# Performance work log

Measured on AMD Instinct MI355X. Metric: run time of the kernel, lower is better.

Reference implementation:

```python
import jax, jax.numpy as jnp
import numpy as np

H = 4096          # hidden_size
NIN = 17          # RFSIZE*RFSIZE + ADDINPUT + NBACTIONS = 9+4+4
NA = 4            # NBACTIONS


def setup_inputs() -> dict:
    key = jax.random.key(0)
    ks = jax.random.split(key, 12)
    return {
        "x": jax.random.normal(ks[0], (1, NIN), jnp.float32),
        "hidden": 0.1 * jax.random.normal(ks[1], (1, H), jnp.float32),
        "hebb": 0.01 * jax.random.normal(ks[2], (H, H), jnp.float32),
        "i2h_w": 0.1 * jax.random.normal(ks[3], (H, NIN), jnp.float32),
        "i2h_b": 0.1 * jax.random.normal(ks[4], (H,), jnp.float32),
        "w": 0.01 * jax.random.uniform(ks[5], (H, H), jnp.float32),
        "alpha": 0.01 * jax.random.uniform(ks[6], (H, H), jnp.float32),
        "eta": 0.01 * jnp.ones((1,), jnp.float32),
        "h2o_w": 0.1 * jax.random.normal(ks[7], (NA, H), jnp.float32),
        "h2o_b": 0.1 * jax.random.normal(ks[8], (NA,), jnp.float32),
        "h2v_w": 0.1 * jax.random.normal(ks[9], (1, H), jnp.float32),
        "h2v_b": 0.1 * jax.random.normal(ks[10], (1,), jnp.float32),
    }


def reference(x, hidden, hebb, i2h_w, i2h_b, w, alpha, eta, h2o_w, h2o_b, h2v_w, h2v_b):
    # plastic RNN step: h = tanh(i2h(x) + hidden @ (w + alpha*hebb))
    h = jnp.tanh(x @ i2h_w.T + i2h_b + hidden @ (w + alpha * hebb))  # [1,H]
    # Hebbian trace update: (1-eta)*hebb + eta * outer(hidden, h)
    hebb_new = (1.0 - eta) * hebb + eta * (hidden[0][:, None] * h[0][None, :])  # [H,H]
    activout = jax.nn.softmax(h @ h2o_w.T + h2o_b, axis=-1)  # [1,NA]
    valueout = h @ h2v_w.T + h2v_b                           # [1,1]
    return activout, valueout, h, hebb_new
```

## Files before the change

### kernel.cpp

```cpp
#include <hip/hip_runtime.h>

#define HDIM 4096
#define NIN 17
#define NA 4

using f4 = __attribute__((ext_vector_type(4))) float;

constexpr int TB = 256;
constexpr int CPT = 4;
constexpr int BXC = HDIM / (TB * CPT);
constexpr int NCHUNK = 512;
constexpr int RPC = HDIM / NCHUNK;
constexpr size_t NELEM = (size_t)HDIM * HDIM;

__global__ __launch_bounds__(TB, 2)
void k_matvec(const float* __restrict__ w, const float* __restrict__ alpha,
              const float* __restrict__ hebb, const float* __restrict__ hidden,
              float* __restrict__ partial, float* __restrict__ acc5,
              unsigned* __restrict__ cnt) {
    if (blockIdx.x == 0 && blockIdx.y == 0 && threadIdx.x < 9) {
        if (threadIdx.x < 8) acc5[threadIdx.x] = 0.f;
        else *cnt = 0u;
    }
    const int col0 = (blockIdx.x * TB + threadIdx.x) * CPT;
    const int row0 = blockIdx.y * RPC;
    const size_t base = (size_t)row0 * HDIM + col0;

    f4 wv[RPC], av[RPC], bv[RPC];
#pragma unroll
    for (int r = 0; r < RPC; ++r) {
        const size_t off = base + (size_t)r * HDIM;
        wv[r] = __builtin_nontemporal_load((const f4*)(w + off));
        av[r] = __builtin_nontemporal_load((const f4*)(alpha + off));
        bv[r] = *(const f4*)(hebb + off);
    }
    __builtin_amdgcn_sched_barrier(0);

    f4 acc = {0.f, 0.f, 0.f, 0.f};
#pragma unroll
    for (int r = 0; r < RPC; ++r) {
        const float hv = hidden[row0 + r];
        acc += hv * (wv[r] + av[r] * bv[r]);
    }
    *(f4*)(partial + (size_t)blockIdx.y * HDIM + col0) = acc;
}

constexpr int HC = 32;
constexpr int HGRP = TB / HC;
constexpr int HCPG = NCHUNK / HGRP;

__global__ void k_hact(const float* __restrict__ partial, const float* __restrict__ x,
                       const float* __restrict__ i2h_w, const float* __restrict__ i2h_b,
                       const float* __restrict__ h2o_w, const float* __restrict__ h2o_b,
                       const float* __restrict__ h2v_w, const float* __restrict__ h2v_b,
                       float* __restrict__ h_f, float* __restrict__ h_out,
                       float* __restrict__ acc5, unsigned* __restrict__ cnt,
                       float* __restrict__ out) {
    const int tid = threadIdx.x;
    const int lane = tid & (HC - 1);
    const int grp = tid >> 5;
    const int col = blockIdx.x * HC + lane;

    float s = 0.f;
    const float* p = partial + (size_t)(grp * HCPG) * HDIM + col;
#pragma unroll 16
    for (int c = 0; c < HCPG; ++c) s += p[(size_t)c * HDIM];

    __shared__ float red[TB];
    red[tid] = s;
    __syncthreads();
    for (int st = TB / 2; st >= HC; st >>= 1) {
        if (tid < st) red[tid] += red[tid + st];
        __syncthreads();
    }
    if (tid < HC) {
        float z = red[tid] + i2h_b[col];
#pragma unroll
        for (int k = 0; k < NIN; ++k) z += x[k] * i2h_w[col * NIN + k];
        const float h = tanhf(z);
        h_f[col] = h;
        h_out[col] = h;
        float d[NA + 1];
#pragma unroll
        for (int a = 0; a < NA; ++a) d[a] = h * h2o_w[(size_t)a * HDIM + col];
        d[NA] = h * h2v_w[col];
#pragma unroll
        for (int a = 0; a <= NA; ++a) {
            float v = d[a];
#pragma unroll
            for (int sft = 16; sft > 0; sft >>= 1) v += __shfl_down(v, sft, 32);
            if (lane == 0) atomicAdd(acc5 + a, v);
        }
    }
    if (tid == 0) {
        __threadfence();
        if (atomicAdd(cnt, 1u) == (HDIM / HC) - 1) {
            float res[NA + 1];
#pragma unroll
            for (int a = 0; a <= NA; ++a) res[a] = atomicAdd(acc5 + a, 0.f);
            float o[NA];
            float mx = -1e30f;
#pragma unroll
            for (int a = 0; a < NA; ++a) { o[a] = res[a] + h2o_b[a]; mx = fmaxf(mx, o[a]); }
            float se = 0.f;
#pragma unroll
            for (int a = 0; a < NA; ++a) { o[a] = __expf(o[a] - mx); se += o[a]; }
#pragma unroll
            for (int a = 0; a < NA; ++a) out[a] = o[a] / se;
            out[NA] = res[NA] + h2v_b[0];
        }
    }
}

constexpr size_t NQK = (NELEM - 4) / 4;
constexpr int HEB_BLK = 4096;

__global__ void k_hebb(const float* __restrict__ hebb, const float* __restrict__ hidden,
                       const float* __restrict__ h_f, const float* __restrict__ eta,
                       float* __restrict__ hebb_out) {
    const int tid = threadIdx.x;
    const size_t gt = (size_t)blockIdx.x * TB + tid;
    const size_t wid = gt >> 6;
    const int lane = tid & 63;
    const float e = eta[0];
    const float om = 1.f - e;

    if (gt == 0) {
        const float hv0 = e * hidden[0];
        hebb_out[0] = om * hebb[0] + hv0 * h_f[0];
        hebb_out[1] = om * hebb[1] + hv0 * h_f[1];
        hebb_out[2] = om * hebb[2] + hv0 * h_f[2];
        hebb_out[NELEM - 1] = om * hebb[NELEM - 1] + e * hidden[HDIM - 1] * h_f[HDIM - 1];
    }

    size_t k[4];
    bool ok[4];
    f4 A[4];
#pragma unroll
    for (int q = 0; q < 4; ++q) {
        k[q] = wid * 256 + (size_t)lane + (size_t)q * 64;
        ok[q] = k[q] < NQK;
        A[q] = *(const f4*)(hebb + 4 * k[q]);
    }
    __builtin_amdgcn_sched_barrier(0);

    f4 B[4];
#pragma unroll
    for (int q = 0; q < 4; ++q) {
        B[q].x = __shfl_down(A[q].x, 1, 64);
        B[q].y = __shfl_down(A[q].y, 1, 64);
        B[q].z = __shfl_down(A[q].z, 1, 64);
        B[q].w = 0.f;
    }
    if (lane == 63) {
#pragma unroll
        for (int q = 0; q < 4; ++q)
            if (ok[q]) B[q] = *(const f4*)(hebb + 4 * (k[q] + 1));
    }

#pragma unroll
    for (int q = 0; q < 4; ++q) {
        if (ok[q]) {
            const size_t s = 4 * k[q] + 3;
            const float b[4] = {A[q].w, B[q].x, B[q].y, B[q].z};
            f4 v;
#pragma unroll
            for (int kk = 0; kk < 4; ++kk) {
                const size_t m = s + (size_t)kk;
                const int i = (int)(m >> 12);
                const int jj = (int)(m & (HDIM - 1));
                v[kk] = om * b[kk] + e * hidden[i] * h_f[jj];
            }
            __builtin_nontemporal_store(v, (f4*)(hebb_out + s));
        }
    }
}

extern "C" void kernel_launch(void* const* d_in, const int* in_sizes, int n_in,
                              void* d_out, int out_size, void* d_ws, size_t ws_size,
                              hipStream_t stream) {
    const float* x      = (const float*)d_in[0];
    const float* hidden = (const float*)d_in[1];
    const float* hebb   = (const float*)d_in[2];
    const float* i2h_w  = (const float*)d_in[3];
    const float* i2h_b  = (const float*)d_in[4];
    const float* w      = (const float*)d_in[5];
    const float* alpha  = (const float*)d_in[6];
    const float* eta    = (const float*)d_in[7];
    const float* h2o_w  = (const float*)d_in[8];
    const float* h2o_b  = (const float*)d_in[9];
    const float* h2v_w  = (const float*)d_in[10];
    const float* h2v_b  = (const float*)d_in[11];
    float* out = (float*)d_out;

    float* h_out    = out + 5;
    float* hebb_out = out + 5 + HDIM;

    float* partial = out + 8192;

    float* h_f  = (float*)d_ws;
    float* acc5 = h_f + HDIM;
    unsigned* cnt = (unsigned*)(acc5 + 8);

    k_matvec<<<dim3(BXC, NCHUNK), TB, 0, stream>>>(w, alpha, hebb, hidden, partial, acc5, cnt);
    k_hact<<<HDIM / HC, TB, 0, stream>>>(partial, x, i2h_w, i2h_b, h2o_w, h2o_b,
                                         h2v_w, h2v_b, h_f, h_out, acc5, cnt, out);
    k_hebb<<<HEB_BLK, TB, 0, stream>>>(hebb, hidden, h_f, eta, hebb_out);
}
```

Before: 259.6 us.

## Restructure matvec so each block covers full rows with looped accumulation

```diff
diff --git a/kernel.cpp b/kernel.cpp
--- a/kernel.cpp
+++ b/kernel.cpp
@@ -7,42 +7,42 @@
 using f4 = __attribute__((ext_vector_type(4))) float;
 
 constexpr int TB = 256;
-constexpr int CPT = 4;
-constexpr int BXC = HDIM / (TB * CPT);
 constexpr int NCHUNK = 512;
 constexpr int RPC = HDIM / NCHUNK;
 constexpr size_t NELEM = (size_t)HDIM * HDIM;
 
-__global__ __launch_bounds__(TB, 2)
+__global__ __launch_bounds__(TB)
 void k_matvec(const float* __restrict__ w, const float* __restrict__ alpha,
               const float* __restrict__ hebb, const float* __restrict__ hidden,
               float* __restrict__ partial, float* __restrict__ acc5,
               unsigned* __restrict__ cnt) {
-    if (blockIdx.x == 0 && blockIdx.y == 0 && threadIdx.x < 9) {
+    if (blockIdx.x == 0 && threadIdx.x < 9) {
         if (threadIdx.x < 8) acc5[threadIdx.x] = 0.f;
         else *cnt = 0u;
     }
-    const int col0 = (blockIdx.x * TB + threadIdx.x) * CPT;
-    const int row0 = blockIdx.y * RPC;
-    const size_t base = (size_t)row0 * HDIM + col0;
-
-    f4 wv[RPC], av[RPC], bv[RPC];
-#pragma unroll
+    const int tid = threadIdx.x;
+    const int row0 = blockIdx.x * RPC;
+    const int c0 = tid * 4;
+
+    f4 acc[4] = {{0.f,0.f,0.f,0.f},{0.f,0.f,0.f,0.f},{0.f,0.f,0.f,0.f},{0.f,0.f,0.f,0.f}};
+#pragma unroll 2
     for (int r = 0; r < RPC; ++r) {
-        const size_t off = base + (size_t)r * HDIM;
-        wv[r] = __builtin_nontemporal_load((const f4*)(w + off));
-        av[r] = __builtin_nontemporal_load((const f4*)(alpha + off));
-        bv[r] = *(const f4*)(hebb + off);
-    }
-    __builtin_amdgcn_sched_barrier(0);
-
-    f4 acc = {0.f, 0.f, 0.f, 0.f};
-#pragma unroll
-    for (int r = 0; r < RPC; ++r) {
-        const float hv = hidden[row0 + r];
-        acc += hv * (wv[r] + av[r] * bv[r]);
-    }
-    *(f4*)(partial + (size_t)blockIdx.y * HDIM + col0) = acc;
+        const int i = row0 + r;
+        const float hv = hidden[i];
+        const size_t rb = (size_t)i * HDIM;
+#pragma unroll
+        for (int q = 0; q < 4; ++q) {
+            const size_t off = rb + (size_t)q * 1024 + c0;
+            const f4 wv = __builtin_nontemporal_load((const f4*)(w + off));
+            const f4 av = __builtin_nontemporal_load((const f4*)(alpha + off));
+            const f4 bv = *(const f4*)(hebb + off);
+            acc[q] += hv * (wv + av * bv);
+        }
+    }
+    float* pb = partial + (size_t)blockIdx.x * HDIM;
+#pragma unroll
+    for (int q = 0; q < 4; ++q)
+        *(f4*)(pb + (size_t)q * 1024 + c0) = acc[q];
 }
 
 constexpr int HC = 32;
@@ -202,7 +202,7 @@
     float* acc5 = h_f + HDIM;
     unsigned* cnt = (unsigned*)(acc5 + 8);
 
-    k_matvec<<<dim3(BXC, NCHUNK), TB, 0, stream>>>(w, alpha, hebb, hidden, partial, acc5, cnt);
+    k_matvec<<<NCHUNK, TB, 0, stream>>>(w, alpha, hebb, hidden, partial, acc5, cnt);
     k_hact<<<HDIM / HC, TB, 0, stream>>>(partial, x, i2h_w, i2h_b, h2o_w, h2o_b,
                                          h2v_w, h2v_b, h_f, h_out, acc5, cnt, out);
     k_hebb<<<HEB_BLK, TB, 0, stream>>>(hebb, hidden, h_f, eta, hebb_out);
```

Result: no change. 260.1 us (+0.2%).
